# Optimization experiments

Measured on AMD Instinct MI355X. Metric: run time of the kernel, lower is better.

## Reference

```python
import jax, jax.numpy as jnp
import numpy as np

EMBED = 128
HEADS = 32          # embed_dim // 4, forced by fuse Conv2d channel counts
HEAD_DIM = EMBED // HEADS  # 4
WS = (4, 7, 7)
N = WS[0] * WS[1] * WS[2]  # 196 tokens per window
B = 64              # batch * num_windows
SCALE = HEAD_DIM ** -0.5
EPS = 1e-5


def _rel_index():
    d, h, w = WS
    coords = np.stack(np.meshgrid(np.arange(d), np.arange(h), np.arange(w), indexing='ij'))
    flat = coords.reshape(3, -1)                       # [3, N]
    rel = (flat[:, :, None] - flat[:, None, :]).transpose(1, 2, 0).astype(np.int64)  # [N,N,3]
    rel[:, :, 0] += d - 1
    rel[:, :, 1] += h - 1
    rel[:, :, 2] += w - 1
    rel[:, :, 0] *= (2 * h - 1) * (2 * w - 1)
    rel[:, :, 1] *= (2 * w - 1)
    return rel.sum(-1).astype(np.int32)                # [N, N]


def setup_inputs() -> dict:
    key = jax.random.key(0)
    ks = jax.random.split(key, 7)
    d, h, w = WS
    tbl = (2 * d - 1) * (2 * h - 1) * (2 * w - 1)
    return {
        'x_in':      jax.random.normal(ks[0], (B, N, EMBED), dtype=jnp.float32),
        'x_in2':     jax.random.normal(ks[1], (B, N, EMBED), dtype=jnp.float32),
        'qkv_w':     jax.random.normal(ks[2], (3 * EMBED, EMBED), dtype=jnp.float32) * 0.02,
        'proj_w':    jax.random.normal(ks[3], (EMBED, EMBED), dtype=jnp.float32) * 0.02,
        'proj_b':    jnp.zeros((EMBED,), dtype=jnp.float32),
        'rpb_table': jax.random.normal(ks[4], (tbl, HEADS), dtype=jnp.float32) * 0.02,
        'fuse_w':    jax.random.normal(ks[5], (EMBED // 4, EMBED // 2), dtype=jnp.float32) * 0.1,
        'fuse_b':    jnp.zeros((EMBED // 4,), dtype=jnp.float32),
        'rel_idx':   jnp.asarray(_rel_index()),
    }


def _branch(x, qkv_w):
    b, n, c = x.shape
    qkv = (x @ qkv_w.T).reshape(b, n, 3, HEADS, c // HEADS).transpose(2, 0, 3, 1, 4)
    q, k, v = qkv[0] * SCALE, qkv[1], qkv[2]           # [b, H, n, d]
    attn = jnp.einsum('bhnd,bhmd->bhnm', q, k)         # [b, H, n, n]
    return attn, v


def reference(x_in, x_in2, qkv_w, proj_w, proj_b, rpb_table, fuse_w, fuse_b, rel_idx):
    b, n, c = x_in.shape
    attn1, v1 = _branch(x_in, qkv_w)
    attn2, v2 = _branch(x_in2, qkv_w)

    # conv-gated value fusion: Conv2d 1x1 over channel dim (= 2H) + InstanceNorm2d + ReLU + Sigmoid
    vcat = jnp.concatenate([v1, v2], axis=1)           # [b, 2H, n, d]
    v = jnp.einsum('bcnd,oc->bond', vcat, fuse_w) + fuse_b[None, :, None, None]  # [b, H, n, d]
    mu = v.mean(axis=(2, 3), keepdims=True)
    var = v.var(axis=(2, 3), keepdims=True)            # biased, as InstanceNorm2d
    v = (v - mu) * jax.lax.rsqrt(var + EPS)
    v = jax.nn.sigmoid(jax.nn.relu(v))

    # relative position bias: gather [n*n] rows of table -> [H, n, n]
    bias = rpb_table[rel_idx[:n, :n].reshape(-1)].reshape(n, n, HEADS).transpose(2, 0, 1)

    attn = jax.nn.softmax(attn1 + attn2 + bias[None], axis=-1)  # [b, H, n, n]
    x = jnp.einsum('bhnm,bhmd->bhnd', attn, v).transpose(0, 2, 1, 3).reshape(b, n, c)
    return x @ proj_w.T + proj_b
```

## Files before the change

kernel.cpp:

```cpp
#include <hip/hip_runtime.h>
#include <hip/hip_bf16.h>
#include <stdint.h>

#define NB   64
#define NTOK 196
#define NH   32
#define HD   4
#define CE   128
#define NM   38416

typedef __bf16 bf16x8 __attribute__((ext_vector_type(8)));
typedef short  bf16x4s __attribute__((ext_vector_type(4)));
typedef float  f32x4  __attribute__((ext_vector_type(4)));

#define QSCALE 0.7213475204444817f
#define LOG2E  1.4426950408889634f

__device__ __forceinline__ float u2f(unsigned short u) {
    union { unsigned int i; float f; } z;
    z.i = ((unsigned int)u) << 16;
    return z.f;
}
__device__ __forceinline__ unsigned short f2u(float f) {
    union { float f; unsigned int i; } z; z.f = f;
    unsigned int x = z.i;
    return (unsigned short)((x + 0x7fffu + ((x >> 16) & 1u)) >> 16);
}

extern "C" __global__ __launch_bounds__(256) void qkv_bias(
    const float* __restrict__ x1,
    const float* __restrict__ x2,
    const float* __restrict__ qkvw,
    const int* __restrict__ rel_idx, const float* __restrict__ rpb,
    unsigned short* __restrict__ Qb, unsigned short* __restrict__ Kb,
    unsigned short* __restrict__ V, unsigned short* __restrict__ biasM)
{
    __shared__ alignas(16) unsigned short AT[64][136];
    __shared__ alignas(16) unsigned short BT[64][136];
    const int tid = threadIdx.x;

    if (blockIdx.y == 6) {
        const int bx = blockIdx.x;
        const int qt = bx % 13, h = bx / 13;
        const int lane = tid & 63, wv = tid >> 6;
        const int quad = lane >> 4, tc = lane & 15;
        for (int nt = wv; nt < 14; nt += 4) {
            union { uint2 v; unsigned short s[4]; } e;
#pragma unroll
            for (int r = 0; r < 4; ++r) {
                int q   = qt * 16 + tc;
                int key = nt * 16 + quad * 4 + r;
                unsigned short u = 0xFF80;
                if (q < 196 && key < 196) {
                    int idx = rel_idx[q * 196 + key];
                    u = f2u(rpb[idx * 32 + h] * LOG2E);
                }
                e.s[r] = u;
            }
            unsigned int off = (((h * 13 + qt) * 7 + (nt >> 1)) * 64 + lane) * 8
                               + (nt & 1) * 4;
            *(uint2*)(biasM + off) = e.v;
        }
        return;
    }
    if (blockIdx.x >= 392) return;

    const int r0 = blockIdx.x * 64;
    const int j0 = blockIdx.y * 64;

    for (int idx = tid; idx < 2048; idx += 256) {
        int row = idx >> 5, k0 = (idx & 31) << 2;
        int r = r0 + row;
        const float* xp = (r >= 12544) ? x2 : x1;
        int rem = r - ((r >= 12544) ? 12544 : 0);
        float4 v = *(const float4*)&xp[rem * 128 + k0];
        ushort4 u; u.x = f2u(v.x); u.y = f2u(v.y); u.z = f2u(v.z); u.w = f2u(v.w);
        *(ushort4*)&AT[row][k0] = u;
    }
    for (int idx = tid; idx < 2048; idx += 256) {
        int row = idx >> 5, k0 = (idx & 31) << 2;
        float4 v = *(const float4*)&qkvw[(j0 + row) * 128 + k0];
        ushort4 u; u.x = f2u(v.x); u.y = f2u(v.y); u.z = f2u(v.z); u.w = f2u(v.w);
        *(ushort4*)&BT[row][k0] = u;
    }
    __syncthreads();

    const int lane = tid & 63, w = tid >> 6;
    const int wj = (w >> 1) * 32;
    const int wt = (w & 1) * 32;
    const int quad = lane >> 4, tc = lane & 15;

    f32x4 acc[2][2] = {};
#pragma unroll
    for (int ks = 0; ks < 4; ++ks) {
        int k0 = ks * 32 + quad * 8;
        bf16x8 a0 = *(const bf16x8*)&BT[wj + tc][k0];
        bf16x8 a1 = *(const bf16x8*)&BT[wj + 16 + tc][k0];
        bf16x8 b0 = *(const bf16x8*)&AT[wt + tc][k0];
        bf16x8 b1 = *(const bf16x8*)&AT[wt + 16 + tc][k0];
        acc[0][0] = __builtin_amdgcn_mfma_f32_16x16x32_bf16(a0, b0, acc[0][0], 0, 0, 0);
        acc[0][1] = __builtin_amdgcn_mfma_f32_16x16x32_bf16(a0, b1, acc[0][1], 0, 0, 0);
        acc[1][0] = __builtin_amdgcn_mfma_f32_16x16x32_bf16(a1, b0, acc[1][0], 0, 0, 0);
        acc[1][1] = __builtin_amdgcn_mfma_f32_16x16x32_bf16(a1, b1, acc[1][1], 0, 0, 0);
    }

    const int sel = j0 >> 7;
#pragma unroll
    for (int mi = 0; mi < 2; ++mi) {
        int jbase = (j0 + wj + mi * 16 + quad * 4) & 127;
        int hh = jbase >> 2;
#pragma unroll
        for (int ni = 0; ni < 2; ++ni) {
            int tok = r0 + wt + ni * 16 + tc;
            int branch = (tok >= 12544) ? 1 : 0;
            int rem = tok - branch * 12544;
            int bb = rem / 196;
            int nn = rem - bb * 196;
            union { uint2 v; unsigned short s[4]; } pk2;
            if (sel == 0) {
#pragma unroll
                for (int r = 0; r < 4; ++r) pk2.s[r] = f2u(acc[mi][ni][r] * QSCALE);
                *(uint2*)&Qb[((bb * 32 + hh) * 196 + nn) * 8 + branch * 4] = pk2.v;
            } else if (sel == 1) {
#pragma unroll
                for (int r = 0; r < 4; ++r) pk2.s[r] = f2u(acc[mi][ni][r]);
                *(uint2*)&Kb[((bb * 32 + hh) * 196 + nn) * 8 + branch * 4] = pk2.v;
            } else {
#pragma unroll
                for (int r = 0; r < 4; ++r) pk2.s[r] = f2u(acc[mi][ni][r]);
                *(uint2*)&V[(bb * 64 + branch * 32 + hh) * 784 + nn * 4] = pk2.v;
            }
        }
    }
}

__device__ __forceinline__ float block_sum(float v, float* red, int tid) {
#pragma unroll
    for (int off = 32; off > 0; off >>= 1) v += __shfl_down(v, off);
    __syncthreads();
    if ((tid & 63) == 0) red[tid >> 6] = v;
    __syncthreads();
    return red[0] + red[1] + red[2] + red[3];
}

__device__ __forceinline__ float act_sig_relu(float x) {
    return x > 0.f ? __fdividef(1.f, 1.f + __expf(-x)) : 0.5f;
}

extern "C" __global__ __launch_bounds__(256) void attn_kernel(
    const unsigned short* __restrict__ Qb, const unsigned short* __restrict__ Kb,
    const unsigned short* __restrict__ V, const float* __restrict__ fuse_w,
    const float* __restrict__ fuse_b, const unsigned short* __restrict__ biasM,
    unsigned short* __restrict__ Ob)
{
    const int bh = blockIdx.x;
    const int b = bh >> 5, h = bh & 31;
    __shared__ alignas(16) unsigned short Qs[208][8];
    __shared__ alignas(16) unsigned short Ks[224][8];
    __shared__ alignas(16) unsigned short VT[16][232];
    __shared__ float fws[64];
    __shared__ float red[4];
    const int tid = threadIdx.x;

    const unsigned short* Qrow = Qb + bh * 196 * 8;
    const unsigned short* Krow = Kb + bh * 196 * 8;
    if (tid < 208) {
        uint4 z = {0, 0, 0, 0};
        uint4 v = (tid < 196) ? *(const uint4*)(Qrow + tid * 8) : z;
        *(uint4*)&Qs[tid][0] = v;
    }
    if (tid < 224) {
        uint4 z = {0, 0, 0, 0};
        uint4 v = (tid < 196) ? *(const uint4*)(Krow + tid * 8) : z;
        *(uint4*)&Ks[tid][0] = v;
    }
    {
        unsigned int* vtw = (unsigned int*)&VT[0][0];
        for (int i = tid; i < (16 * 232) / 2; i += 256) vtw[i] = 0u;
    }
    if (tid < 64) fws[tid] = fuse_w[h * 64 + tid];
    __syncthreads();

    const unsigned short* Vb = V + b * 64 * 784;
    float a0 = 0.f, a1 = 0.f, a2 = 0.f, t0 = 0.f;
    const bool tail = tid < 16;
    for (int c = 0; c < 64; ++c) {
        float w0 = fws[c];
        const unsigned short* Vc = Vb + c * 784;
        a0 = fmaf(w0, u2f(Vc[tid]),       a0);
        a1 = fmaf(w0, u2f(Vc[tid + 256]), a1);
        a2 = fmaf(w0, u2f(Vc[tid + 512]), a2);
        if (tail) t0 = fmaf(w0, u2f(Vc[tid + 768]), t0);
    }
    float fb0 = fuse_b[h];
    a0 += fb0; a1 += fb0; a2 += fb0; t0 += fb0;

    float s_  = a0 + a1 + a2 + (tail ? t0 : 0.f);
    float q_  = a0*a0 + a1*a1 + a2*a2 + (tail ? t0*t0 : 0.f);
    float S0 = block_sum(s_, red, tid);
    float Q0 = block_sum(q_, red, tid);
    const float inv784 = 1.0f / 784.0f;
    float mu = S0 * inv784;
    float rstd = rsqrtf(Q0 * inv784 - mu * mu + 1e-5f);

    {
        float vals[4] = { act_sig_relu((a0 - mu) * rstd),
                          act_sig_relu((a1 - mu) * rstd),
                          act_sig_relu((a2 - mu) * rstd),
                          act_sig_relu((t0 - mu) * rstd) };
#pragma unroll
        for (int k = 0; k < 3; ++k) {
            int nd = tid + 256 * k;
            VT[nd & 3][nd >> 2] = f2u(vals[k]);
            if ((nd & 3) == 0) VT[4][nd >> 2] = 0x3F80;
        }
        if (tail) {
            int nd = tid + 768;
            VT[nd & 3][nd >> 2] = f2u(vals[3]);
            if ((nd & 3) == 0) VT[4][nd >> 2] = 0x3F80;
        }
    }
    __syncthreads();

    const int lane = tid & 63, wv = tid >> 6;
    const int quad = lane >> 4, tc = lane & 15;

    bf16x4s vfr16[14];
#pragma unroll
    for (int t = 0; t < 14; ++t)
        vfr16[t] = *(const bf16x4s*)&VT[tc][t * 16 + quad * 4];

    const unsigned short* bias_h = biasM + (unsigned)(h * 13) * 3584;

    for (int qt = wv; qt < 13; qt += 4) {
        bf16x8 bq = {};
        if (quad == 0) bq = *(const bf16x8*)&Qs[qt * 16 + tc][0];
        const unsigned short* bias_q = bias_h + qt * 3584;
        uint4 bw[7];
#pragma unroll
        for (int kt = 0; kt < 7; ++kt)
            bw[kt] = *(const uint4*)(bias_q + kt * 512 + lane * 8);
        f32x4 O0 = {}, O1 = {};
#pragma unroll
        for (int kt = 0; kt < 7; ++kt) {
            f32x4 s0, s1;
            {
                union { unsigned int u; float f; } c;
                c.u = bw[kt].x << 16;          s0[0] = c.f;
                c.u = bw[kt].x & 0xffff0000u;  s0[1] = c.f;
                c.u = bw[kt].y << 16;          s0[2] = c.f;
                c.u = bw[kt].y & 0xffff0000u;  s0[3] = c.f;
                c.u = bw[kt].z << 16;          s1[0] = c.f;
                c.u = bw[kt].z & 0xffff0000u;  s1[1] = c.f;
                c.u = bw[kt].w << 16;          s1[2] = c.f;
                c.u = bw[kt].w & 0xffff0000u;  s1[3] = c.f;
            }
            bf16x8 ka0 = *(const bf16x8*)&Ks[(kt * 2 + 0) * 16 + tc][0];
            bf16x8 ka1 = *(const bf16x8*)&Ks[(kt * 2 + 1) * 16 + tc][0];
            s0 = __builtin_amdgcn_mfma_f32_16x16x32_bf16(ka0, bq, s0, 0, 0, 0);
            s1 = __builtin_amdgcn_mfma_f32_16x16x32_bf16(ka1, bq, s1, 0, 0, 0);
            float e0 = __builtin_amdgcn_exp2f(s0[0]);
            float e1 = __builtin_amdgcn_exp2f(s0[1]);
            float e2 = __builtin_amdgcn_exp2f(s0[2]);
            float e3 = __builtin_amdgcn_exp2f(s0[3]);
            float g0 = __builtin_amdgcn_exp2f(s1[0]);
            float g1 = __builtin_amdgcn_exp2f(s1[1]);
            float g2 = __builtin_amdgcn_exp2f(s1[2]);
            float g3 = __builtin_amdgcn_exp2f(s1[3]);
            union { int d[2]; bf16x4s v; } pf0, pf1;
            pf0.d[0] = (int)__builtin_amdgcn_perm(__float_as_uint(e1), __float_as_uint(e0), 0x07060302u);
            pf0.d[1] = (int)__builtin_amdgcn_perm(__float_as_uint(e3), __float_as_uint(e2), 0x07060302u);
            pf1.d[0] = (int)__builtin_amdgcn_perm(__float_as_uint(g1), __float_as_uint(g0), 0x07060302u);
            pf1.d[1] = (int)__builtin_amdgcn_perm(__float_as_uint(g3), __float_as_uint(g2), 0x07060302u);
            O0 = __builtin_amdgcn_mfma_f32_16x16x16bf16_1k(vfr16[kt * 2 + 0], pf0.v, O0, 0, 0, 0);
            O1 = __builtin_amdgcn_mfma_f32_16x16x16bf16_1k(vfr16[kt * 2 + 1], pf1.v, O1, 0, 0, 0);
        }
        f32x4 Oacc;
        Oacc[0] = O0[0] + O1[0];
        Oacc[1] = O0[1] + O1[1];
        Oacc[2] = O0[2] + O1[2];
        Oacc[3] = O0[3] + O1[3];
        float rs = __shfl(Oacc[0], 16 + tc);
        int q = qt * 16 + tc;
        if (quad == 0 && q < 196) {
            float inv = __builtin_amdgcn_rcpf(rs);
            union { uint2 v; unsigned short s[4]; } pk2;
            pk2.s[0] = f2u(Oacc[0] * inv);
            pk2.s[1] = f2u(Oacc[1] * inv);
            pk2.s[2] = f2u(Oacc[2] * inv);
            pk2.s[3] = f2u(Oacc[3] * inv);
            *(uint2*)&Ob[(b * 196 + q) * 128 + h * 4] = pk2.v;
        }
    }
}

extern "C" __global__ __launch_bounds__(256) void proj_kernel(
    const unsigned short* __restrict__ Ob, const float* __restrict__ projw,
    const float* __restrict__ projb, float* __restrict__ out)
{
    __shared__ alignas(16) unsigned short AT[64][136];
    __shared__ alignas(16) unsigned short BT[64][136];
    const int tid = threadIdx.x;
    const int r0 = blockIdx.x * 64;
    const int j0 = blockIdx.y * 64;

    for (int idx = tid; idx < 1024; idx += 256) {
        int row = idx >> 4, k0 = (idx & 15) << 3;
        *(uint4*)&AT[row][k0] = *(const uint4*)&Ob[(r0 + row) * 128 + k0];
    }
    for (int idx = tid; idx < 2048; idx += 256) {
        int row = idx >> 5, k0 = (idx & 31) << 2;
        float4 v = *(const float4*)&projw[(j0 + row) * 128 + k0];
        ushort4 u; u.x = f2u(v.x); u.y = f2u(v.y); u.z = f2u(v.z); u.w = f2u(v.w);
        *(ushort4*)&BT[row][k0] = u;
    }
    __syncthreads();

    const int lane = tid & 63, w = tid >> 6;
    const int wm = (w >> 1) * 32, wn = (w & 1) * 32;
    const int quad = lane >> 4, tcol = lane & 15;

    f32x4 acc[2][2] = {};
#pragma unroll
    for (int ks = 0; ks < 4; ++ks) {
        int k0 = ks * 32 + quad * 8;
        bf16x8 a0 = *(const bf16x8*)&AT[wm + tcol][k0];
        bf16x8 a1 = *(const bf16x8*)&AT[wm + 16 + tcol][k0];
        bf16x8 b0 = *(const bf16x8*)&BT[wn + tcol][k0];
        bf16x8 b1 = *(const bf16x8*)&BT[wn + 16 + tcol][k0];
        acc[0][0] = __builtin_amdgcn_mfma_f32_16x16x32_bf16(a0, b0, acc[0][0], 0, 0, 0);
        acc[0][1] = __builtin_amdgcn_mfma_f32_16x16x32_bf16(a0, b1, acc[0][1], 0, 0, 0);
        acc[1][0] = __builtin_amdgcn_mfma_f32_16x16x32_bf16(a1, b0, acc[1][0], 0, 0, 0);
        acc[1][1] = __builtin_amdgcn_mfma_f32_16x16x32_bf16(a1, b1, acc[1][1], 0, 0, 0);
    }

#pragma unroll
    for (int mi = 0; mi < 2; ++mi) {
#pragma unroll
        for (int ni = 0; ni < 2; ++ni) {
            int j = j0 + wn + ni * 16 + tcol;
            float pb = projb[j];
#pragma unroll
            for (int reg = 0; reg < 4; ++reg) {
                int r = r0 + wm + mi * 16 + quad * 4 + reg;
                out[r * 128 + j] = acc[mi][ni][reg] + pb;
            }
        }
    }
}

extern "C" void kernel_launch(void* const* d_in, const int* in_sizes, int n_in,
                              void* d_out, int out_size, void* d_ws, size_t ws_size,
                              hipStream_t stream)
{
    const float* x1    = (const float*)d_in[0];
    const float* x2    = (const float*)d_in[1];
    const float* qkvw  = (const float*)d_in[2];
    const float* projw = (const float*)d_in[3];
    const float* projb = (const float*)d_in[4];
    const float* rpb   = (const float*)d_in[5];
    const float* fw    = (const float*)d_in[6];
    const float* fb    = (const float*)d_in[7];
    const int*   rel   = (const int*)d_in[8];
    float* out = (float*)d_out;

    char* w = (char*)d_ws;
    unsigned short* Qb  = (unsigned short*)(w);
    unsigned short* Kb  = (unsigned short*)(w + 6422528);
    unsigned short* V   = (unsigned short*)(w + 12845056);
    unsigned short* bM  = (unsigned short*)(w + 19267584);
    unsigned short* Ob  = (unsigned short*)(w + 22249472);

    qkv_bias  <<<dim3(416, 7), dim3(256), 0, stream>>>(x1, x2, qkvw, rel, rpb,
                                                       Qb, Kb, V, bM);
    attn_kernel<<<dim3(2048),   dim3(256), 0, stream>>>(Qb, Kb, V, fw, fb, bM, Ob);
    proj_kernel<<<dim3(196, 2), dim3(256), 0, stream>>>(Ob, projw, projb, out);
}
```

Before: 175.4 us.

## Split value fusion and instance-norm into a separate kernel ahead of attention

Moves the 1x1 conv value fusion, InstanceNorm, and ReLU/sigmoid out of attn_kernel into a new fuse_kernel. Each fuse_kernel block handles four output heads, so every V load is reused across four weights. Before, each (batch, head) attention block re-read all 64 V channels, and that work was repeated 32 times per batch. The change adds a kernel launch plus an fp32 Vf round trip through global memory. It also shortens attn_kernel's prologue and frees registers and LDS there.

```diff
diff --git a/kernel.cpp b/kernel.cpp
--- a/kernel.cpp
+++ b/kernel.cpp
@@ -147,10 +147,68 @@
     return x > 0.f ? __fdividef(1.f, 1.f + __expf(-x)) : 0.5f;
 }
 
+extern "C" __global__ __launch_bounds__(256) void fuse_kernel(
+    const unsigned short* __restrict__ V,
+    const float* __restrict__ fuse_w,
+    const float* __restrict__ fuse_b,
+    float* __restrict__ Vf)
+{
+    const int b = blockIdx.x, o0 = blockIdx.y * 4;
+    const int tid = threadIdx.x;
+    __shared__ float fws[4][64];
+    __shared__ float red[4];
+    fws[tid >> 6][tid & 63] = fuse_w[(o0 + (tid >> 6)) * 64 + (tid & 63)];
+    __syncthreads();
+
+    const bool act = tid < 196;
+    const unsigned short* Vb = V + b * 64 * 784 + tid * 4;
+    float4 a[4] = {};
+    for (int c = 0; c < 64; ++c) {
+        float4 x = {0.f, 0.f, 0.f, 0.f};
+        if (act) {
+            uint2 u = *(const uint2*)(Vb + c * 784);
+            union { unsigned int i; float f; } z;
+            z.i = u.x << 16;          x.x = z.f;
+            z.i = u.x & 0xffff0000u;  x.y = z.f;
+            z.i = u.y << 16;          x.z = z.f;
+            z.i = u.y & 0xffff0000u;  x.w = z.f;
+        }
+#pragma unroll
+        for (int o = 0; o < 4; ++o) {
+            float w0 = fws[o][c];
+            a[o].x = fmaf(w0, x.x, a[o].x);
+            a[o].y = fmaf(w0, x.y, a[o].y);
+            a[o].z = fmaf(w0, x.z, a[o].z);
+            a[o].w = fmaf(w0, x.w, a[o].w);
+        }
+    }
+
+    const float inv784 = 1.0f / 784.0f;
+#pragma unroll
+    for (int o = 0; o < 4; ++o) {
+        float fb0 = fuse_b[o0 + o];
+        float4 v = a[o];
+        if (act) { v.x += fb0; v.y += fb0; v.z += fb0; v.w += fb0; }
+        float s = v.x + v.y + v.z + v.w;
+        float q = v.x*v.x + v.y*v.y + v.z*v.z + v.w*v.w;
+        float S = block_sum(s, red, tid);
+        float Q = block_sum(q, red, tid);
+        float mu = S * inv784;
+        float rstd = rsqrtf(Q * inv784 - mu * mu + 1e-5f);
+        if (act) {
+            float4 o4;
+            o4.x = act_sig_relu((v.x - mu) * rstd);
+            o4.y = act_sig_relu((v.y - mu) * rstd);
+            o4.z = act_sig_relu((v.z - mu) * rstd);
+            o4.w = act_sig_relu((v.w - mu) * rstd);
+            *(float4*)&Vf[(b * 32 + o0 + o) * 784 + tid * 4] = o4;
+        }
+    }
+}
+
 extern "C" __global__ __launch_bounds__(256) void attn_kernel(
     const unsigned short* __restrict__ Qb, const unsigned short* __restrict__ Kb,
-    const unsigned short* __restrict__ V, const float* __restrict__ fuse_w,
-    const float* __restrict__ fuse_b, const unsigned short* __restrict__ biasM,
+    const float* __restrict__ Vf, const unsigned short* __restrict__ biasM,
     unsigned short* __restrict__ Ob)
 {
     const int bh = blockIdx.x;
@@ -158,8 +216,6 @@
     __shared__ alignas(16) unsigned short Qs[208][8];
     __shared__ alignas(16) unsigned short Ks[224][8];
     __shared__ alignas(16) unsigned short VT[16][232];
-    __shared__ float fws[64];
-    __shared__ float red[4];
     const int tid = threadIdx.x;
 
     const unsigned short* Qrow = Qb + bh * 196 * 8;
@@ -178,47 +234,12 @@
         unsigned int* vtw = (unsigned int*)&VT[0][0];
         for (int i = tid; i < (16 * 232) / 2; i += 256) vtw[i] = 0u;
     }
-    if (tid < 64) fws[tid] = fuse_w[h * 64 + tid];
-    __syncthreads();
-
-    const unsigned short* Vb = V + b * 64 * 784;
-    float a0 = 0.f, a1 = 0.f, a2 = 0.f, t0 = 0.f;
-    const bool tail = tid < 16;
-    for (int c = 0; c < 64; ++c) {
-        float w0 = fws[c];
-        const unsigned short* Vc = Vb + c * 784;
-        a0 = fmaf(w0, u2f(Vc[tid]),       a0);
-        a1 = fmaf(w0, u2f(Vc[tid + 256]), a1);
-        a2 = fmaf(w0, u2f(Vc[tid + 512]), a2);
-        if (tail) t0 = fmaf(w0, u2f(Vc[tid + 768]), t0);
-    }
-    float fb0 = fuse_b[h];
-    a0 += fb0; a1 += fb0; a2 += fb0; t0 += fb0;
-
-    float s_  = a0 + a1 + a2 + (tail ? t0 : 0.f);
-    float q_  = a0*a0 + a1*a1 + a2*a2 + (tail ? t0*t0 : 0.f);
-    float S0 = block_sum(s_, red, tid);
-    float Q0 = block_sum(q_, red, tid);
-    const float inv784 = 1.0f / 784.0f;
-    float mu = S0 * inv784;
-    float rstd = rsqrtf(Q0 * inv784 - mu * mu + 1e-5f);
-
-    {
-        float vals[4] = { act_sig_relu((a0 - mu) * rstd),
-                          act_sig_relu((a1 - mu) * rstd),
-                          act_sig_relu((a2 - mu) * rstd),
-                          act_sig_relu((t0 - mu) * rstd) };
-#pragma unroll
-        for (int k = 0; k < 3; ++k) {
-            int nd = tid + 256 * k;
-            VT[nd & 3][nd >> 2] = f2u(vals[k]);
-            if ((nd & 3) == 0) VT[4][nd >> 2] = 0x3F80;
-        }
-        if (tail) {
-            int nd = tid + 768;
-            VT[nd & 3][nd >> 2] = f2u(vals[3]);
-            if ((nd & 3) == 0) VT[4][nd >> 2] = 0x3F80;
-        }
+    __syncthreads();
+    if (tid < 196) {
+        float4 vv = *(const float4*)(Vf + bh * 784 + tid * 4);
+        VT[0][tid] = f2u(vv.x); VT[1][tid] = f2u(vv.y);
+        VT[2][tid] = f2u(vv.z); VT[3][tid] = f2u(vv.w);
+        VT[4][tid] = 0x3F80;
     }
     __syncthreads();
 
@@ -368,11 +389,13 @@
     unsigned short* Qb  = (unsigned short*)(w);
     unsigned short* Kb  = (unsigned short*)(w + 6422528);
     unsigned short* V   = (unsigned short*)(w + 12845056);
-    unsigned short* bM  = (unsigned short*)(w + 19267584);
-    unsigned short* Ob  = (unsigned short*)(w + 22249472);
+    float*          Vf  = (float*)(w + 19267584);
+    unsigned short* bM  = (unsigned short*)(w + 25690112);
+    unsigned short* Ob  = (unsigned short*)(w + 28672000);
 
     qkv_bias  <<<dim3(416, 7), dim3(256), 0, stream>>>(x1, x2, qkvw, rel, rpb,
                                                        Qb, Kb, V, bM);
-    attn_kernel<<<dim3(2048),   dim3(256), 0, stream>>>(Qb, Kb, V, fw, fb, bM, Ob);
+    fuse_kernel<<<dim3(64, 8),  dim3(256), 0, stream>>>(V, fw, fb, Vf);
+    attn_kernel<<<dim3(2048),   dim3(256), 0, stream>>>(Qb, Kb, Vf, bM, Ob);
     proj_kernel<<<dim3(196, 2), dim3(256), 0, stream>>>(Ob, projw, projb, out);
 }
```

Measured after the change: 155.1 us. 1.13x faster.
